# Kernel tuning notes

Hardware: AMD Instinct MI355X
Metric: run time of the kernel (lower is better)

## Reference

```python
import jax, jax.numpy as jnp
import numpy as np

N, E, D, H, ED, L, G = 20000, 320000, 256, 256, 64, 4, 64


def setup_inputs() -> dict:
    key = jax.random.key(0)
    ks = jax.random.split(key, 24)
    w = lambda k, shape: jax.random.normal(k, shape, dtype=jnp.float32) * 0.05
    inp = {
        "x": jax.random.normal(ks[0], (N, D), dtype=jnp.float32),
        "edge_attr": jax.random.normal(ks[1], (E, ED), dtype=jnp.float32),
        "pos": jax.random.normal(ks[2], (N, 3), dtype=jnp.float32),
        "edge_index": jax.random.randint(ks[3], (2, E), 0, N, dtype=jnp.int32),
        "batch": jnp.sort(jax.random.randint(ks[4], (N,), 0, G, dtype=jnp.int32)),
        # stacked per-layer params [L, ...]
        "node_w": w(ks[5], (L, D, H)), "node_b": w(ks[6], (L, H)),
        "edge_w": w(ks[7], (L, ED, H)), "edge_b": w(ks[8], (L, H)),
        "msg_w1": w(ks[9], (L, 2 * H + 1, H)), "msg_b1": w(ks[10], (L, H)),
        "msg_w2": w(ks[11], (L, H, H)), "msg_b2": w(ks[12], (L, H)),
        "upd_w1": w(ks[13], (L, H, H)), "upd_b1": w(ks[14], (L, H)),
        "upd_w2": w(ks[15], (L, H, D)), "upd_b2": w(ks[16], (L, D)),
        # global pooling head
        "fc_w1": w(ks[17], (D, H)), "fc_b1": w(ks[18], (H,)),
        "fc_w2": w(ks[19], (H, 1)), "fc_b2": w(ks[20], (1,)),
    }
    return inp


def reference(x, edge_attr, pos, edge_index, batch,
              node_w, node_b, edge_w, edge_b,
              msg_w1, msg_b1, msg_w2, msg_b2,
              upd_w1, upd_b1, upd_w2, upd_b2,
              fc_w1, fc_b1, fc_w2, fc_b2):
    src = edge_index[0]  # x_j (source / message sender)
    dst = edge_index[1]  # x_i (target / aggregation index)
    # edge distance depends only on fixed pos/edge_index: compute once
    edge_dist = jnp.linalg.norm(pos[src] - pos[dst], axis=1, keepdims=True)  # [E,1]
    silu = jax.nn.silu
    for l in range(L):
        x_emb = x @ node_w[l] + node_b[l]                    # [N,H]
        e_emb = edge_attr @ edge_w[l] + edge_b[l]            # [E,H]
        m_in = jnp.concatenate([x_emb[dst], x_emb[src], edge_dist], axis=-1)  # [E,2H+1]
        m = silu(m_in @ msg_w1[l] + msg_b1[l])
        m = silu(m @ msg_w2[l] + msg_b2[l]) + e_emb          # [E,H]
        aggr = jax.ops.segment_sum(m, dst, num_segments=N)   # scatter-add into target nodes
        x = silu(aggr @ upd_w1[l] + upd_b1[l]) @ upd_w2[l] + upd_b2[l]  # [N,D]
    pooled = jax.ops.segment_sum(x, batch, num_segments=G)   # [G,D]
    out = silu(pooled @ fc_w1 + fc_b1) @ fc_w2 + fc_b2       # [G,1]
    return out
```

## Files before the change

kernel.cpp:

```cpp
#include <hip/hip_runtime.h>
#include <hip/hip_bf16.h>
#include <math.h>

#define N_NODES 20000
#define N_EDGES 320000
#define NGRAPH 64

typedef __attribute__((ext_vector_type(8))) short short8;
typedef __attribute__((ext_vector_type(4))) short short4x;
typedef __attribute__((ext_vector_type(4))) float f32x4;

__device__ __forceinline__ float silu_f(float v){ return v / (1.0f + __expf(-v)); }
__device__ __forceinline__ float bf2f(short s){
  unsigned u = ((unsigned)(unsigned short)s) << 16;
  float f; __builtin_memcpy(&f, &u, 4); return f;
}
__device__ __forceinline__ short f2bf(float f){
  unsigned u; __builtin_memcpy(&u, &f, 4);
  unsigned r = (u + 0x7FFFu + ((u >> 16) & 1u)) >> 16;
  return (short)r;
}

__global__ void k_hist(const int* __restrict__ ei, int* __restrict__ cnt){
  int e = blockIdx.x*256 + threadIdx.x;
  if (e >= N_EDGES) return;
  atomicAdd(&cnt[ei[N_EDGES + e]], 1);
}

__global__ void k_scan(const int* __restrict__ cnt, int* __restrict__ row_ptr,
                       int* __restrict__ off){
  __shared__ int ssum[256];
  int t = threadIdx.x;
  const int CHK = (N_NODES + 255)/256;
  int base = t*CHK;
  int s = 0;
  for(int i=0;i<CHK;i++){ int idx=base+i; if(idx<N_NODES) s += cnt[idx]; }
  ssum[t]=s; __syncthreads();
  for(int o=1;o<256;o<<=1){
    int v = (t>=o)? ssum[t-o] : 0;
    __syncthreads();
    ssum[t] += v;
    __syncthreads();
  }
  int pre = (t==0)? 0 : ssum[t-1];
  for(int i=0;i<CHK;i++){
    int idx=base+i; if(idx>=N_NODES) break;
    row_ptr[idx]=pre; off[idx]=pre; pre += cnt[idx];
  }
  if(t==255) row_ptr[N_NODES]=pre;
}

__global__ void k_scatter(const int* __restrict__ ei, int* __restrict__ off,
                          int* __restrict__ src_s, int* __restrict__ dst_s,
                          int* __restrict__ eid_s){
  int e = blockIdx.x*256 + threadIdx.x;
  if (e >= N_EDGES) return;
  int d = ei[N_EDGES + e];
  int p = atomicAdd(&off[d], 1);
  dst_s[p]=d; src_s[p]=ei[e]; eid_s[p]=e;
}

__global__ void k_dist_s(const int* __restrict__ src_s, const int* __restrict__ dst_s,
                         const float* __restrict__ pos, float* __restrict__ dist_s){
  int i = blockIdx.x*256 + threadIdx.x;
  if (i >= N_EDGES) return;
  int s = src_s[i], d = dst_s[i];
  float dx = pos[s*3+0]-pos[d*3+0];
  float dy = pos[s*3+1]-pos[d*3+1];
  float dz = pos[s*3+2]-pos[d*3+2];
  dist_s[i] = sqrtf(dx*dx+dy*dy+dz*dz);
}

__global__ void k_eaagg_s(const int* __restrict__ row_ptr, const int* __restrict__ eid_s,
                          const float* __restrict__ edge_attr, float* __restrict__ EA){
  int sub = threadIdx.x>>6, j = threadIdx.x&63;
  int d = blockIdx.x*4 + sub;
  if (d >= N_NODES) return;
  int b = row_ptr[d], e = row_ptr[d+1];
  float s = 0.f;
  for(int i=b;i<e;i++) s += edge_attr[(size_t)eid_s[i]*64 + j];
  EA[(size_t)d*96 + j] = s;
  if (j < 32) EA[(size_t)d*96 + 64 + j] = (j==0) ? (float)(e-b) : 0.f;
}

__global__ void k_f2b(const float* __restrict__ S, short* __restrict__ D, int n4){
  int i = blockIdx.x*256 + threadIdx.x;
  if (i >= n4) return;
  float4 v = ((const float4*)S)[i];
  short4x o;
  o[0]=f2bf(v.x); o[1]=f2bf(v.y); o[2]=f2bf(v.z); o[3]=f2bf(v.w);
  ((short4x*)D)[i] = o;
}

__global__ void k_trans5(const float* __restrict__ w1, const float* __restrict__ w2,
                         const float* __restrict__ uw1, const float* __restrict__ uw2,
                         short* __restrict__ w1aT, short* __restrict__ w1bT,
                         short* __restrict__ w2T, short* __restrict__ uw1T,
                         short* __restrict__ uw2T){
  const float* S; short* D;
  switch(blockIdx.z){
    case 0: S=w1;          D=w1aT; break;
    case 1: S=w1+256*256;  D=w1bT; break;
    case 2: S=w2;          D=w2T;  break;
    case 3: S=uw1;         D=uw1T; break;
    default: S=uw2;        D=uw2T; break;
  }
  __shared__ float t[32][33];
  int bx = blockIdx.x*32, by = blockIdx.y*32;
  int lx = threadIdx.x & 31, ly = threadIdx.x >> 5;
  #pragma unroll
  for(int r=0;r<4;r++){ int k = ly + r*8; t[k][lx] = S[(size_t)(by+k)*256 + bx+lx]; }
  __syncthreads();
  #pragma unroll
  for(int r=0;r<4;r++){
    int n = ly + r*8;
    D[(size_t)(bx+n)*256 + by+lx] = f2bf(t[lx][n]);
  }
}

__global__ void k_ewaugT(const float* __restrict__ ew, const float* __restrict__ eb,
                         short* __restrict__ ewT){
  int n = blockIdx.x, c = threadIdx.x;
  float v = (c < 64) ? ew[(size_t)c*256 + n] : (c == 64 ? eb[n] : 0.f);
  ewT[(size_t)n*96 + c] = f2bf(v);
}

__global__ void k_biasm_acc(const float* __restrict__ nb, const float* __restrict__ w1,
                            const float* __restrict__ mb1, float* __restrict__ biasm){
  int j = threadIdx.x;
  int b = blockIdx.x;
  if (b == 16){ atomicAdd(&biasm[j], mb1[j]); return; }
  float s = 0.f;
  for(int k = b*16; k < b*16+16; k++)
    s += nb[k]*(w1[(size_t)k*256+j] + w1[(size_t)(256+k)*256+j]);
  atomicAdd(&biasm[j], s);
}

template<int K_REAL, int K_LDS, int AF32, int BIAS, int ACT, int OF32, int OBF16>
__global__ __launch_bounds__(256)
void k_gemm_mfma(const void* __restrict__ A, const short* __restrict__ BT,
                 const float* __restrict__ bias, float* __restrict__ Cf,
                 short* __restrict__ Cb, int M, int Nld){
  __shared__ __align__(16) short As[32][K_LDS];
  const int CHL = K_LDS/8, CH = K_REAL/8;
  int tid = threadIdx.x;
  int m0 = blockIdx.y*32, n0 = blockIdx.x*256;
  for(int c = tid; c < 32*CHL; c += 256){
    int row = c / CHL, ch = c % CHL;
    short8 v;
    if (ch < CH) {
      if (AF32){
        const float* Af = (const float*)A;
        float4 f0 = *(const float4*)&Af[(size_t)(m0+row)*K_REAL + ch*8];
        float4 f1 = *(const float4*)&Af[(size_t)(m0+row)*K_REAL + ch*8 + 4];
        v[0]=f2bf(f0.x); v[1]=f2bf(f0.y); v[2]=f2bf(f0.z); v[3]=f2bf(f0.w);
        v[4]=f2bf(f1.x); v[5]=f2bf(f1.y); v[6]=f2bf(f1.z); v[7]=f2bf(f1.w);
      } else {
        v = *(const short8*)&((const short*)A)[(size_t)(m0+row)*K_REAL + ch*8];
      }
    } else {
      v = (short8){0,0,0,0,0,0,0,0};
    }
    *(short8*)&As[row][(ch ^ (row&7))*8] = v;
  }
  __syncthreads();
  int wid = tid>>6, lane = tid&63, l15 = lane&15, lq = lane>>4;
  int ncol0 = n0 + wid*64;
  f32x4 acc[2][4];
  #pragma unroll
  for(int mt=0;mt<2;mt++)
    #pragma unroll
    for(int nt=0;nt<4;nt++) acc[mt][nt] = (f32x4){0.f,0.f,0.f,0.f};
  for(int k0=0;k0<K_REAL;k0+=32){
    int kc = k0 + 8*lq;
    short8 a[2], b[4];
    #pragma unroll
    for(int mt=0;mt<2;mt++){
      int row = mt*16 + l15;
      a[mt] = *(const short8*)&As[row][kc ^ ((row&7)<<3)];
    }
    #pragma unroll
    for(int nt=0;nt<4;nt++){
      int col = ncol0 + nt*16 + l15;
      b[nt] = *(const short8*)&BT[(size_t)col*K_REAL + kc];
    }
    #pragma unroll
    for(int mt=0;mt<2;mt++)
      #pragma unroll
      for(int nt=0;nt<4;nt++)
        acc[mt][nt] = __builtin_amdgcn_mfma_f32_16x16x32_bf16(a[mt], b[nt], acc[mt][nt], 0, 0, 0);
  }
  #pragma unroll
  for(int mt=0;mt<2;mt++){
    #pragma unroll
    for(int nt=0;nt<4;nt++){
      int col = ncol0 + nt*16 + l15;
      float bb = BIAS ? bias[col] : 0.f;
      #pragma unroll
      for(int r=0;r<4;r++){
        int row = m0 + mt*16 + lq*4 + r;
        float v = acc[mt][nt][r] + bb;
        if (ACT) v = silu_f(v);
        if (OF32)  Cf[(size_t)row*Nld + col] = v;
        if (OBF16) Cb[(size_t)row*Nld + col] = f2bf(v);
      }
    }
  }
}

__global__ __launch_bounds__(256)
void k_edge_mfma(const short* __restrict__ t_ab,
                 const float* __restrict__ dist_s,
                 const int* __restrict__ src_s, const int* __restrict__ dst_s,
                 const float* __restrict__ w1c, const float* __restrict__ biasm,
                 const short* __restrict__ w2T, const float* __restrict__ b2,
                 float* __restrict__ aggr)
{
  __shared__ __align__(16) unsigned char ulds[256*33*4];
  short (*h)[256] = (short(*)[256])ulds;
  float* outl = (float*)ulds;
  __shared__ int sdst[32], ssrc[32];
  __shared__ float sdist[32];
  int tid = threadIdx.x;
  int e0 = blockIdx.x*32;
  if (tid < 32){
    sdst[tid] = dst_s[e0 + tid];
    ssrc[tid] = src_s[e0 + tid];
    sdist[tid] = dist_s[e0 + tid];
  }
  __syncthreads();
  int wid = tid>>6, lane = tid&63;
  int half = lane>>5, cl = lane&31;
  float wc8[8], bm8[8];
  {
    float4 w0 = *(const float4*)&w1c[8*cl], w1v = *(const float4*)&w1c[8*cl+4];
    float4 b0 = *(const float4*)&biasm[8*cl], b1v = *(const float4*)&biasm[8*cl+4];
    wc8[0]=w0.x; wc8[1]=w0.y; wc8[2]=w0.z; wc8[3]=w0.w;
    wc8[4]=w1v.x; wc8[5]=w1v.y; wc8[6]=w1v.z; wc8[7]=w1v.w;
    bm8[0]=b0.x; bm8[1]=b0.y; bm8[2]=b0.z; bm8[3]=b0.w;
    bm8[4]=b1v.x; bm8[5]=b1v.y; bm8[6]=b1v.z; bm8[7]=b1v.w;
  }
  #pragma unroll
  for(int p=0;p<4;p++){
    int e = wid*8 + p*2 + half;
    int d = sdst[e], s = ssrc[e];
    float de = sdist[e];
    short8 va = *(const short8*)&t_ab[(size_t)d*512 + 8*cl];
    short8 vb = *(const short8*)&t_ab[(size_t)s*512 + 256 + 8*cl];
    short8 hv;
    #pragma unroll
    for(int i=0;i<8;i++){
      float f = bf2f(va[i]) + bf2f(vb[i]) + de*wc8[i] + bm8[i];
      hv[i] = f2bf(silu_f(f));
    }
    *(short8*)&h[e][(8*cl) ^ ((e&7)<<3)] = hv;
  }
  __syncthreads();

  int l15 = lane & 15, lq = lane >> 4;
  int nb = wid*64;
  f32x4 acc[2][4];
  #pragma unroll
  for(int mt=0;mt<2;mt++)
    #pragma unroll
    for(int nt=0;nt<4;nt++) acc[mt][nt] = (f32x4){0.f,0.f,0.f,0.f};

  for(int k0=0;k0<256;k0+=32){
    int kc = k0 + 8*lq;
    short8 a[2], b[4];
    #pragma unroll
    for(int mt=0;mt<2;mt++){
      int row = mt*16 + l15;
      a[mt] = *(const short8*)&h[row][kc ^ ((row&7)<<3)];
    }
    #pragma unroll
    for(int nt=0;nt<4;nt++){
      int col = nb + nt*16 + l15;
      b[nt] = *(const short8*)&w2T[(size_t)col*256 + kc];
    }
    #pragma unroll
    for(int mt=0;mt<2;mt++)
      #pragma unroll
      for(int nt=0;nt<4;nt++)
        acc[mt][nt] = __builtin_amdgcn_mfma_f32_16x16x32_bf16(a[mt], b[nt], acc[mt][nt], 0, 0, 0);
  }
  __syncthreads();

  #pragma unroll
  for(int mt=0;mt<2;mt++){
    #pragma unroll
    for(int nt=0;nt<4;nt++){
      int col = nb + nt*16 + l15;
      float bb = b2[col];
      #pragma unroll
      for(int r=0;r<4;r++){
        int row = mt*16 + lq*4 + r;
        outl[col*33 + row] = silu_f(acc[mt][nt][r] + bb);
      }
    }
  }
  __syncthreads();

  int j = tid;
  float accu = 0.f;
  int prev = sdst[0];
  #pragma unroll
  for(int e=0;e<32;e++){
    int d = sdst[e];
    if (d != prev){
      atomicAdd(&aggr[(size_t)prev*256 + j], accu);
      accu = 0.f; prev = d;
    }
    accu += outl[j*33 + e];
  }
  atomicAdd(&aggr[(size_t)prev*256 + j], accu);
}

__global__ void k_ghist(const int* __restrict__ batch, int* __restrict__ gcnt){
  int n = blockIdx.x*256 + threadIdx.x;
  if (n >= N_NODES) return;
  atomicAdd(&gcnt[batch[n]], 1);
}
__global__ void k_gscan(const int* __restrict__ gcnt, int* __restrict__ gptr){
  if (threadIdx.x == 0){
    int s = 0;
    for(int g=0; g<NGRAPH; g++){ gptr[g]=s; s += gcnt[g]; }
    gptr[NGRAPH] = s;
  }
}
__global__ void k_pool_seg(const float* __restrict__ x, const int* __restrict__ gptr,
                           float* __restrict__ pooled){
  int g = blockIdx.x, j = threadIdx.x;
  int b = gptr[g], e = gptr[g+1];
  float s = 0.f;
  for(int n=b; n<e; n++) s += x[(size_t)n*256 + j];
  pooled[g*256 + j] = s;
}

__global__ void k_head(const float* __restrict__ pooled, const float* __restrict__ fw1,
                       const float* __restrict__ fb1, const float* __restrict__ fw2,
                       const float* __restrict__ fb2, float* __restrict__ out){
  __shared__ float red[256];
  int g = blockIdx.x, j = threadIdx.x;
  float s = fb1[j];
  const float* p = &pooled[g*256];
  for(int k=0;k<256;k++) s += p[k]*fw1[k*256+j];
  float hv = silu_f(s)*fw2[j];
  red[j]=hv; __syncthreads();
  for(int off=128;off>0;off>>=1){ if(j<off) red[j]+=red[j+off]; __syncthreads(); }
  if(j==0) out[g] = red[0] + fb2[0];
}

extern "C" void kernel_launch(void* const* d_in, const int* in_sizes, int n_in,
                              void* d_out, int out_size, void* d_ws, size_t ws_size,
                              hipStream_t stream) {
  const float* x_in      = (const float*)d_in[0];
  const float* edge_attr = (const float*)d_in[1];
  const float* pos       = (const float*)d_in[2];
  const int*   ei        = (const int*)d_in[3];
  const int*   batch     = (const int*)d_in[4];
  const float* node_w    = (const float*)d_in[5];
  const float* node_b    = (const float*)d_in[6];
  const float* edge_w    = (const float*)d_in[7];
  const float* edge_b    = (const float*)d_in[8];
  const float* msg_w1    = (const float*)d_in[9];
  const float* msg_b1    = (const float*)d_in[10];
  const float* msg_w2    = (const float*)d_in[11];
  const float* msg_b2    = (const float*)d_in[12];
  const float* upd_w1    = (const float*)d_in[13];
  const float* upd_b1    = (const float*)d_in[14];
  const float* upd_w2    = (const float*)d_in[15];
  const float* upd_b2    = (const float*)d_in[16];
  const float* fc_w1     = (const float*)d_in[17];
  const float* fc_b1     = (const float*)d_in[18];
  const float* fc_w2     = (const float*)d_in[19];
  const float* fc_b2     = (const float*)d_in[20];
  float* out = (float*)d_out;

  float* ws = (float*)d_ws;
  int* cnt     = (int*)ws; ws += N_NODES;
  int* off     = (int*)ws; ws += N_NODES;
  int* row_ptr = (int*)ws; ws += N_NODES+4;
  int* src_s   = (int*)ws; ws += N_EDGES;
  int* dst_s   = (int*)ws; ws += N_EDGES;
  int* eid_s   = (int*)ws; ws += N_EDGES;
  float* dist_s= ws; ws += N_EDGES;
  int* gcnt    = (int*)ws; ws += NGRAPH;
  int* gptr    = (int*)ws; ws += NGRAPH+4;
  short* x_bf   = (short*)ws; ws += (size_t)N_NODES*256/2;
  float* EA_aug = ws; ws += (size_t)N_NODES*96;
  short* WabT   = (short*)ws; ws += 512*256/2;
  short* w1aT   = (short*)ws; ws += 256*256/2;
  short* w1bT   = (short*)ws; ws += 256*256/2;
  short* w2T    = (short*)ws; ws += 256*256/2;
  short* uw1T   = (short*)ws; ws += 256*256/2;
  short* uw2T   = (short*)ws; ws += 256*256/2;
  short* ewT    = (short*)ws; ws += 256*96/2;
  short* nw_bf  = (short*)ws; ws += 256*256/2;
  float* biasm  = ws; ws += 256;
  float* tabreg = ws; ws += (size_t)N_NODES*256;
  float* aggr   = ws; ws += (size_t)N_NODES*256;
  float* pooled = ws; ws += NGRAPH*256;

  short* t_ab   = (short*)tabreg;
  short* h_bf   = (short*)tabreg;
  float* xfinal = aggr;

  hipMemsetAsync(cnt, 0, N_NODES*sizeof(int), stream);
  k_hist<<<(N_EDGES+255)/256, 256, 0, stream>>>(ei, cnt);
  k_scan<<<1, 256, 0, stream>>>(cnt, row_ptr, off);
  k_scatter<<<(N_EDGES+255)/256, 256, 0, stream>>>(ei, off, src_s, dst_s, eid_s);
  k_dist_s<<<(N_EDGES+255)/256, 256, 0, stream>>>(src_s, dst_s, pos, dist_s);
  k_eaagg_s<<<N_NODES/4, 256, 0, stream>>>(row_ptr, eid_s, edge_attr, EA_aug);
  hipMemsetAsync(gcnt, 0, NGRAPH*sizeof(int), stream);
  k_ghist<<<(N_NODES+255)/256, 256, 0, stream>>>(batch, gcnt);
  k_gscan<<<1, 64, 0, stream>>>(gcnt, gptr);

  for(int l=0;l<4;l++){
    const float* nw  = node_w + (size_t)l*256*256;
    const float* nb  = node_b + l*256;
    const float* w1  = msg_w1 + (size_t)l*513*256;
    const float* mb1 = msg_b1 + l*256;
    const float* w2  = msg_w2 + (size_t)l*256*256;
    const float* mb2 = msg_b2 + l*256;
    const float* ewp = edge_w + (size_t)l*64*256;
    const float* ebp = edge_b + l*256;
    const float* uw1 = upd_w1 + (size_t)l*256*256;
    const float* ub1 = upd_b1 + l*256;
    const float* uw2 = upd_w2 + (size_t)l*256*256;
    const float* ub2 = upd_b2 + l*256;

    k_trans5<<<dim3(8,8,5), 256, 0, stream>>>(w1, w2, uw1, uw2, w1aT, w1bT, w2T, uw1T, uw2T);
    k_ewaugT<<<256, 96, 0, stream>>>(ewp, ebp, ewT);
    k_f2b<<<64, 256, 0, stream>>>(nw, nw_bf, 256*256/4);
    k_gemm_mfma<256,256,0,0,0,0,1><<<dim3(1,8), 256, 0, stream>>>(w1aT, nw_bf, nullptr, nullptr, WabT,         256, 256);
    k_gemm_mfma<256,256,0,0,0,0,1><<<dim3(1,8), 256, 0, stream>>>(w1bT, nw_bf, nullptr, nullptr, WabT+256*256, 256, 256);
    hipMemsetAsync(biasm, 0, 256*sizeof(float), stream);
    k_biasm_acc<<<17, 256, 0, stream>>>(nb, w1, mb1, biasm);

    if (l == 0)
      k_gemm_mfma<256,256,1,0,0,0,1><<<dim3(2,625), 256, 0, stream>>>(x_in, WabT, nullptr, nullptr, t_ab, N_NODES, 512);
    else
      k_gemm_mfma<256,256,0,0,0,0,1><<<dim3(2,625), 256, 0, stream>>>(x_bf, WabT, nullptr, nullptr, t_ab, N_NODES, 512);

    k_gemm_mfma<96,128,1,0,0,1,0><<<dim3(1,625), 256, 0, stream>>>(EA_aug, ewT, nullptr, aggr, nullptr, N_NODES, 256);

    k_edge_mfma<<<N_EDGES/32, 256, 0, stream>>>(t_ab, dist_s, src_s, dst_s,
                                                w1 + 512*256, biasm, w2T, mb2, aggr);

    k_gemm_mfma<256,256,1,1,1,0,1><<<dim3(1,625), 256, 0, stream>>>(aggr, uw1T, ub1, nullptr, h_bf, N_NODES, 256);
    if (l < 3)
      k_gemm_mfma<256,256,0,1,0,0,1><<<dim3(1,625), 256, 0, stream>>>(h_bf, uw2T, ub2, nullptr, x_bf, N_NODES, 256);
    else
      k_gemm_mfma<256,256,0,1,0,1,0><<<dim3(1,625), 256, 0, stream>>>(h_bf, uw2T, ub2, xfinal, nullptr, N_NODES, 256);
  }

  k_pool_seg<<<NGRAPH, 256, 0, stream>>>(xfinal, gptr, pooled);
  k_head<<<NGRAPH, 256, 0, stream>>>(pooled, fc_w1, fc_b1, fc_w2, fc_b2, out);
}
```

Baseline: 1.381 ms.

## Batch per-layer weight prep across layers and shrink edge-kernel LDS

All per-layer weight transposes, bf16 conversions, the combined W_ab GEMMs and the fused bias sums now run once before the layer loop, using blockIdx.z/y to cover the four layers. This replaces roughly 28 small launches inside the loop with about 6. The edge kernel's output staging is split into two 16-edge halves, which halves its LDS footprint and may allow higher occupancy at the cost of extra barriers. Each lane now handles consecutive edges, so the destination row is reloaded only when the destination changes.

```diff
diff --git a/kernel.cpp b/kernel.cpp
--- a/kernel.cpp
+++ b/kernel.cpp
@@ -92,19 +92,19 @@
   ((short4x*)D)[i] = o;
 }
 
-__global__ void k_trans5(const float* __restrict__ w1, const float* __restrict__ w2,
-                         const float* __restrict__ uw1, const float* __restrict__ uw2,
-                         short* __restrict__ w1aT, short* __restrict__ w1bT,
-                         short* __restrict__ w2T, short* __restrict__ uw1T,
-                         short* __restrict__ uw2T){
-  const float* S; short* D;
-  switch(blockIdx.z){
-    case 0: S=w1;          D=w1aT; break;
-    case 1: S=w1+256*256;  D=w1bT; break;
-    case 2: S=w2;          D=w2T;  break;
-    case 3: S=uw1;         D=uw1T; break;
-    default: S=uw2;        D=uw2T; break;
-  }
+__global__ void k_transW(const float* __restrict__ msg_w1, const float* __restrict__ msg_w2,
+                         const float* __restrict__ upd_w1, const float* __restrict__ upd_w2,
+                         short* __restrict__ wT){
+  int z = blockIdx.z; int l = z/5, w = z%5;
+  const float* S;
+  switch(w){
+    case 0: S = msg_w1 + (size_t)l*513*256; break;
+    case 1: S = msg_w1 + (size_t)l*513*256 + 256*256; break;
+    case 2: S = msg_w2 + (size_t)l*256*256; break;
+    case 3: S = upd_w1 + (size_t)l*256*256; break;
+    default: S = upd_w2 + (size_t)l*256*256; break;
+  }
+  short* D = wT + (size_t)z*65536;
   __shared__ float t[32][33];
   int bx = blockIdx.x*32, by = blockIdx.y*32;
   int lx = threadIdx.x & 31, ly = threadIdx.x >> 5;
@@ -118,18 +118,23 @@
   }
 }
 
-__global__ void k_ewaugT(const float* __restrict__ ew, const float* __restrict__ eb,
-                         short* __restrict__ ewT){
-  int n = blockIdx.x, c = threadIdx.x;
+__global__ void k_ewaugT(const float* __restrict__ edge_w, const float* __restrict__ edge_b,
+                         short* __restrict__ ewT4){
+  int n = blockIdx.x, c = threadIdx.x, l = blockIdx.y;
+  const float* ew = edge_w + (size_t)l*64*256;
+  const float* eb = edge_b + l*256;
   float v = (c < 64) ? ew[(size_t)c*256 + n] : (c == 64 ? eb[n] : 0.f);
-  ewT[(size_t)n*96 + c] = f2bf(v);
-}
-
-__global__ void k_biasm_acc(const float* __restrict__ nb, const float* __restrict__ w1,
-                            const float* __restrict__ mb1, float* __restrict__ biasm){
+  ewT4[(size_t)l*24576 + (size_t)n*96 + c] = f2bf(v);
+}
+
+__global__ void k_biasm_acc(const float* __restrict__ node_b, const float* __restrict__ msg_w1,
+                            const float* __restrict__ msg_b1, float* __restrict__ biasm4){
   int j = threadIdx.x;
-  int b = blockIdx.x;
-  if (b == 16){ atomicAdd(&biasm[j], mb1[j]); return; }
+  int b = blockIdx.x, l = blockIdx.y;
+  const float* nb  = node_b + l*256;
+  const float* w1  = msg_w1 + (size_t)l*513*256;
+  float* biasm = biasm4 + l*256;
+  if (b == 16){ atomicAdd(&biasm[j], msg_b1[l*256+j]); return; }
   float s = 0.f;
   for(int k = b*16; k < b*16+16; k++)
     s += nb[k]*(w1[(size_t)k*256+j] + w1[(size_t)(256+k)*256+j]);
@@ -140,23 +145,27 @@
 __global__ __launch_bounds__(256)
 void k_gemm_mfma(const void* __restrict__ A, const short* __restrict__ BT,
                  const float* __restrict__ bias, float* __restrict__ Cf,
-                 short* __restrict__ Cb, int M, int Nld){
+                 short* __restrict__ Cb, int M, int Nld,
+                 int AzStr, int BzStr, int CzStr){
   __shared__ __align__(16) short As[32][K_LDS];
   const int CHL = K_LDS/8, CH = K_REAL/8;
   int tid = threadIdx.x;
+  int zz = blockIdx.z;
+  const short* Ab = (const short*)A + (size_t)zz*AzStr;
+  const float* Af = (const float*)A + (size_t)zz*AzStr;
+  BT += (size_t)zz*BzStr;
   int m0 = blockIdx.y*32, n0 = blockIdx.x*256;
   for(int c = tid; c < 32*CHL; c += 256){
     int row = c / CHL, ch = c % CHL;
     short8 v;
     if (ch < CH) {
       if (AF32){
-        const float* Af = (const float*)A;
         float4 f0 = *(const float4*)&Af[(size_t)(m0+row)*K_REAL + ch*8];
         float4 f1 = *(const float4*)&Af[(size_t)(m0+row)*K_REAL + ch*8 + 4];
         v[0]=f2bf(f0.x); v[1]=f2bf(f0.y); v[2]=f2bf(f0.z); v[3]=f2bf(f0.w);
         v[4]=f2bf(f1.x); v[5]=f2bf(f1.y); v[6]=f2bf(f1.z); v[7]=f2bf(f1.w);
       } else {
-        v = *(const short8*)&((const short*)A)[(size_t)(m0+row)*K_REAL + ch*8];
+        v = *(const short8*)&Ab[(size_t)(m0+row)*K_REAL + ch*8];
       }
     } else {
       v = (short8){0,0,0,0,0,0,0,0};
@@ -201,8 +210,8 @@
         int row = m0 + mt*16 + lq*4 + r;
         float v = acc[mt][nt][r] + bb;
         if (ACT) v = silu_f(v);
-        if (OF32)  Cf[(size_t)row*Nld + col] = v;
-        if (OBF16) Cb[(size_t)row*Nld + col] = f2bf(v);
+        if (OF32)  Cf[(size_t)zz*CzStr + (size_t)row*Nld + col] = v;
+        if (OBF16) Cb[(size_t)zz*CzStr + (size_t)row*Nld + col] = f2bf(v);
       }
     }
   }
@@ -216,7 +225,7 @@
                  const short* __restrict__ w2T, const float* __restrict__ b2,
                  float* __restrict__ aggr)
 {
-  __shared__ __align__(16) unsigned char ulds[256*33*4];
+  __shared__ __align__(16) unsigned char ulds[256*17*4];
   short (*h)[256] = (short(*)[256])ulds;
   float* outl = (float*)ulds;
   __shared__ int sdst[32], ssrc[32];
@@ -240,13 +249,19 @@
     bm8[0]=b0.x; bm8[1]=b0.y; bm8[2]=b0.z; bm8[3]=b0.w;
     bm8[4]=b1v.x; bm8[5]=b1v.y; bm8[6]=b1v.z; bm8[7]=b1v.w;
   }
+  int ebase = wid*8 + half*4;
+  int dprev = -1;
+  short8 va;
   #pragma unroll
   for(int p=0;p<4;p++){
-    int e = wid*8 + p*2 + half;
+    int e = ebase + p;
     int d = sdst[e], s = ssrc[e];
+    if (d != dprev){
+      va = *(const short8*)&t_ab[(size_t)d*512 + 8*cl];
+      dprev = d;
+    }
+    short8 vb = *(const short8*)&t_ab[(size_t)s*512 + 256 + 8*cl];
     float de = sdist[e];
-    short8 va = *(const short8*)&t_ab[(size_t)d*512 + 8*cl];
-    short8 vb = *(const short8*)&t_ab[(size_t)s*512 + 256 + 8*cl];
     short8 hv;
     #pragma unroll
     for(int i=0;i<8;i++){
@@ -286,6 +301,9 @@
   }
   __syncthreads();
 
+  int j = tid;
+  float accu = 0.f;
+  int prev = sdst[0];
   #pragma unroll
   for(int mt=0;mt<2;mt++){
     #pragma unroll
@@ -294,24 +312,21 @@
       float bb = b2[col];
       #pragma unroll
       for(int r=0;r<4;r++){
-        int row = mt*16 + lq*4 + r;
-        outl[col*33 + row] = silu_f(acc[mt][nt][r] + bb);
+        int row = lq*4 + r;
+        outl[col*17 + row] = silu_f(acc[mt][nt][r] + bb);
       }
     }
-  }
-  __syncthreads();
-
-  int j = tid;
-  float accu = 0.f;
-  int prev = sdst[0];
-  #pragma unroll
-  for(int e=0;e<32;e++){
-    int d = sdst[e];
-    if (d != prev){
-      atomicAdd(&aggr[(size_t)prev*256 + j], accu);
-      accu = 0.f; prev = d;
-    }
-    accu += outl[j*33 + e];
+    __syncthreads();
+    #pragma unroll
+    for(int e2=0;e2<16;e2++){
+      int d = sdst[mt*16 + e2];
+      if (d != prev){
+        atomicAdd(&aggr[(size_t)prev*256 + j], accu);
+        accu = 0.f; prev = d;
+      }
+      accu += outl[j*17 + e2];
+    }
+    __syncthreads();
   }
   atomicAdd(&aggr[(size_t)prev*256 + j], accu);
 }
@@ -387,17 +402,13 @@
   float* dist_s= ws; ws += N_EDGES;
   int* gcnt    = (int*)ws; ws += NGRAPH;
   int* gptr    = (int*)ws; ws += NGRAPH+4;
+  short* wT     = (short*)ws; ws += 20*65536/2;
+  short* nw_bf4 = (short*)ws; ws += 4*65536/2;
+  short* ewT4   = (short*)ws; ws += 4*24576/2;
+  short* WabT4  = (short*)ws; ws += 4*131072/2;
+  float* biasm4 = ws; ws += 4*256;
   short* x_bf   = (short*)ws; ws += (size_t)N_NODES*256/2;
   float* EA_aug = ws; ws += (size_t)N_NODES*96;
-  short* WabT   = (short*)ws; ws += 512*256/2;
-  short* w1aT   = (short*)ws; ws += 256*256/2;
-  short* w1bT   = (short*)ws; ws += 256*256/2;
-  short* w2T    = (short*)ws; ws += 256*256/2;
-  short* uw1T   = (short*)ws; ws += 256*256/2;
-  short* uw2T   = (short*)ws; ws += 256*256/2;
-  short* ewT    = (short*)ws; ws += 256*96/2;
-  short* nw_bf  = (short*)ws; ws += 256*256/2;
-  float* biasm  = ws; ws += 256;
   float* tabreg = ws; ws += (size_t)N_NODES*256;
   float* aggr   = ws; ws += (size_t)N_NODES*256;
   float* pooled = ws; ws += NGRAPH*256;
@@ -416,43 +427,47 @@
   k_ghist<<<(N_NODES+255)/256, 256, 0, stream>>>(batch, gcnt);
   k_gscan<<<1, 64, 0, stream>>>(gcnt, gptr);
 
+  k_transW<<<dim3(8,8,20), 256, 0, stream>>>(msg_w1, msg_w2, upd_w1, upd_w2, wT);
+  k_ewaugT<<<dim3(256,4), 96, 0, stream>>>(edge_w, edge_b, ewT4);
+  k_f2b<<<256, 256, 0, stream>>>(node_w, nw_bf4, 4*65536/4);
+  hipMemsetAsync(biasm4, 0, 4*256*sizeof(float), stream);
+  k_biasm_acc<<<dim3(17,4), 256, 0, stream>>>(node_b, msg_w1, msg_b1, biasm4);
+  k_gemm_mfma<256,256,0,0,0,0,1><<<dim3(1,8,4), 256, 0, stream>>>(
+      wT,          nw_bf4, nullptr, nullptr, WabT4,         256, 256, 5*65536, 65536, 131072);
+  k_gemm_mfma<256,256,0,0,0,0,1><<<dim3(1,8,4), 256, 0, stream>>>(
+      wT + 65536,  nw_bf4, nullptr, nullptr, WabT4 + 65536, 256, 256, 5*65536, 65536, 131072);
+
   for(int l=0;l<4;l++){
-    const float* nw  = node_w + (size_t)l*256*256;
-    const float* nb  = node_b + l*256;
     const float* w1  = msg_w1 + (size_t)l*513*256;
-    const float* mb1 = msg_b1 + l*256;
-    const float* w2  = msg_w2 + (size_t)l*256*256;
     const float* mb2 = msg_b2 + l*256;
-    const float* ewp = edge_w + (size_t)l*64*256;
-    const float* ebp = edge_b + l*256;
-    const float* uw1 = upd_w1 + (size_t)l*256*256;
     const float* ub1 = upd_b1 + l*256;
-    const float* uw2 = upd_w2 + (size_t)l*256*256;
     const float* ub2 = upd_b2 + l*256;
-
-    k_trans5<<<dim3(8,8,5), 256, 0, stream>>>(w1, w2, uw1, uw2, w1aT, w1bT, w2T, uw1T, uw2T);
-    k_ewaugT<<<256, 96, 0, stream>>>(ewp, ebp, ewT);
-    k_f2b<<<64, 256, 0, stream>>>(nw, nw_bf, 256*256/4);
-    k_gemm_mfma<256,256,0,0,0,0,1><<<dim3(1,8), 256, 0, stream>>>(w1aT, nw_bf, nullptr, nullptr, WabT,         256, 256);
-    k_gemm_mfma<256,256,0,0,0,0,1><<<dim3(1,8), 256, 0, stream>>>(w1bT, nw_bf, nullptr, nullptr, WabT+256*256, 256, 256);
-    hipMemsetAsync(biasm, 0, 256*sizeof(float), stream);
-    k_biasm_acc<<<17, 256, 0, stream>>>(nb, w1, mb1, biasm);
+    const short* w2T_l  = wT + (size_t)(l*5+2)*65536;
+    const short* uw1T_l = wT + (size_t)(l*5+3)*65536;
+    const short* uw2T_l = wT + (size_t)(l*5+4)*65536;
 
     if (l == 0)
-      k_gemm_mfma<256,256,1,0,0,0,1><<<dim3(2,625), 256, 0, stream>>>(x_in, WabT, nullptr, nullptr, t_ab, N_NODES, 512);
+      k_gemm_mfma<256,256,1,0,0,0,1><<<dim3(2,625), 256, 0, stream>>>(
+          x_in, WabT4 + (size_t)l*131072, nullptr, nullptr, t_ab, N_NODES, 512, 0,0,0);
     else
-      k_gemm_mfma<256,256,0,0,0,0,1><<<dim3(2,625), 256, 0, stream>>>(x_bf, WabT, nullptr, nullptr, t_ab, N_NODES, 512);
-
-    k_gemm_mfma<96,128,1,0,0,1,0><<<dim3(1,625), 256, 0, stream>>>(EA_aug, ewT, nullptr, aggr, nullptr, N_NODES, 256);
+      k_gemm_mfma<256,256,0,0,0,0,1><<<dim3(2,625), 256, 0, stream>>>(
+          x_bf, WabT4 + (size_t)l*131072, nullptr, nullptr, t_ab, N_NODES, 512, 0,0,0);
+
+    k_gemm_mfma<96,128,1,0,0,1,0><<<dim3(1,625), 256, 0, stream>>>(
+        EA_aug, ewT4 + (size_t)l*24576, nullptr, aggr, nullptr, N_NODES, 256, 0,0,0);
 
     k_edge_mfma<<<N_EDGES/32, 256, 0, stream>>>(t_ab, dist_s, src_s, dst_s,
-                                                w1 + 512*256, biasm, w2T, mb2, aggr);
-
-    k_gemm_mfma<256,256,1,1,1,0,1><<<dim3(1,625), 256, 0, stream>>>(aggr, uw1T, ub1, nullptr, h_bf, N_NODES, 256);
+                                                w1 + 512*256, biasm4 + l*256,
+                                                w2T_l, mb2, aggr);
+
+    k_gemm_mfma<256,256,1,1,1,0,1><<<dim3(1,625), 256, 0, stream>>>(
+        aggr, uw1T_l, ub1, nullptr, h_bf, N_NODES, 256, 0,0,0);
     if (l < 3)
-      k_gemm_mfma<256,256,0,1,0,0,1><<<dim3(1,625), 256, 0, stream>>>(h_bf, uw2T, ub2, nullptr, x_bf, N_NODES, 256);
+      k_gemm_mfma<256,256,0,1,0,0,1><<<dim3(1,625), 256, 0, stream>>>(
+          h_bf, uw2T_l, ub2, nullptr, x_bf, N_NODES, 256, 0,0,0);
     else
-      k_gemm_mfma<256,256,0,1,0,1,0><<<dim3(1,625), 256, 0, stream>>>(h_bf, uw2T, ub2, xfinal, nullptr, N_NODES, 256);
+      k_gemm_mfma<256,256,0,1,0,1,0><<<dim3(1,625), 256, 0, stream>>>(
+          h_bf, uw2T_l, ub2, xfinal, nullptr, N_NODES, 256, 0,0,0);
   }
 
   k_pool_seg<<<NGRAPH, 256, 0, stream>>>(xfinal, gptr, pooled);
```

Measured after the change: 1.399 ms. Within noise of the previous version (+1.3%).
